# Kernel tuning notes

Measured on AMD Instinct MI355X. Metric: run time of the kernel, lower is better.

Reference implementation:

```python
import jax, jax.numpy as jnp
import numpy as np


@jax.custom_vjp
def sign_ste(x):
    return jnp.sign(x)

def _sign_ste_fwd(x):
    return jnp.sign(x), x

def _sign_ste_bwd(x, g):
    gate = (jnp.abs(x) < 1.0).astype(g.dtype)
    return (g * gate,)

sign_ste.defvjp(_sign_ste_fwd, _sign_ste_bwd)


def setup_inputs() -> dict:
    key = jax.random.key(0)
    ks = jax.random.split(key, 6)
    B, S, D_IN, D_OUT, R = 4, 4096, 4096, 4096, 128
    x = jax.random.normal(ks[0], (B, S, D_IN), dtype=jnp.float32)
    U_latent = jax.random.normal(ks[1], (D_OUT, R), dtype=jnp.float32) * 0.05
    V_latent = jax.random.normal(ks[2], (D_IN, R), dtype=jnp.float32) * 0.05
    s1 = jax.random.uniform(ks[3], (D_OUT,), dtype=jnp.float32, minval=0.01, maxval=0.1)
    s2 = jax.random.uniform(ks[4], (D_IN,), dtype=jnp.float32, minval=0.01, maxval=0.1)
    bias = jax.random.normal(ks[5], (D_OUT,), dtype=jnp.float32) * 0.02
    return {"x": x, "U_latent": U_latent, "V_latent": V_latent, "s1": s1, "s2": s2, "bias": bias}


def reference(x, U_latent, V_latent, s1, s2, bias):
    cdtype = x.dtype
    U_sign = sign_ste(U_latent.astype(cdtype))  # [d_out, r]
    V_sign = sign_ste(V_latent.astype(cdtype))  # [d_in, r]
    z = x * s2.astype(cdtype)                   # [..., d_in]
    z = z @ V_sign                               # [..., r]
    z = z @ U_sign.T                             # [..., d_out]
    z = z * s1.astype(cdtype)
    z = z + bias.astype(cdtype)
    return z
```

## Files before the change

kernel.cpp:

```cpp
#include <hip/hip_runtime.h>

typedef float f32x4 __attribute__((ext_vector_type(4)));
typedef _Float16 f16x8 __attribute__((ext_vector_type(8)));
typedef __fp16 fp16x2 __attribute__((ext_vector_type(2)));

#define M_TOT 16384
#define K_IN  4096
#define R_DIM 128
#define N_OUT 4096

__device__ __forceinline__ _Float16 sign_f16(float v) {
  return v > 0.f ? (_Float16)1.f : (v < 0.f ? (_Float16)-1.f : (_Float16)0.f);
}

__device__ __forceinline__ void cvt8v(f32x4 a, f32x4 b, f16x8& h, f16x8& l) {
#pragma unroll
  for (int j = 0; j < 2; ++j) {
    fp16x2 h0 = __builtin_amdgcn_cvt_pkrtz(a[2 * j], a[2 * j + 1]);
    fp16x2 h1 = __builtin_amdgcn_cvt_pkrtz(b[2 * j], b[2 * j + 1]);
    fp16x2 l0 = __builtin_amdgcn_cvt_pkrtz(a[2 * j] - (float)h0[0], a[2 * j + 1] - (float)h0[1]);
    fp16x2 l1 = __builtin_amdgcn_cvt_pkrtz(b[2 * j] - (float)h1[0], b[2 * j + 1] - (float)h1[1]);
    h[2 * j] = (_Float16)h0[0]; h[2 * j + 1] = (_Float16)h0[1];
    h[4 + 2 * j] = (_Float16)h1[0]; h[5 + 2 * j] = (_Float16)h1[1];
    l[2 * j] = (_Float16)l0[0]; l[2 * j + 1] = (_Float16)l0[1];
    l[4 + 2 * j] = (_Float16)l1[0]; l[5 + 2 * j] = (_Float16)l1[1];
  }
}

__device__ __forceinline__ void gload16(const void* g, void* l) {
  __builtin_amdgcn_global_load_lds((const __attribute__((address_space(1))) unsigned int*)g,
                                   (__attribute__((address_space(3))) unsigned int*)l, 16, 0, 0);
}

__global__ __launch_bounds__(256)
void k_prep(const float* __restrict__ U, const float* __restrict__ V,
            _Float16* __restrict__ VsT_sw, _Float16* __restrict__ Us) {
  __shared__ _Float16 tl[128 * 72];
  const int t = threadIdx.x;
  const int b = blockIdx.x;

  {
    size_t base = (size_t)b * 2048 + (size_t)t * 8;
    f32x4 u0 = *(const f32x4*)(U + base);
    f32x4 u1 = *(const f32x4*)(U + base + 4);
    f16x8 s;
#pragma unroll
    for (int j = 0; j < 4; ++j) { s[j] = sign_f16(u0[j]); s[j + 4] = sign_f16(u1[j]); }
    *(f16x8*)(Us + base) = s;
  }

  if (b < 64) {
#pragma unroll
    for (int it = 0; it < 8; ++it) {
      int idx4 = it * 256 + t;
      int kl = idx4 >> 5;
      int r4 = (idx4 & 31) * 4;
      f32x4 v = *(const f32x4*)(V + (size_t)(b * 64 + kl) * R_DIM + r4);
#pragma unroll
      for (int j = 0; j < 4; ++j) tl[(r4 + j) * 72 + kl] = sign_f16(v[j]);
    }
    __syncthreads();
#pragma unroll
    for (int c = 0; c < 4; ++c) {
      int off = t * 64 + c * 16;
      int r = off >> 7;
      int cB = (off & 127) ^ ((r & 7) << 4);
      f16x8 o = *(const f16x8*)(tl + r * 72 + (cB >> 1));
      *(f16x8*)((char*)VsT_sw + (size_t)b * 16384 + off) = o;
    }
  }
}

#define LOADX(T, X0, X1, X2, X3, S0, S1, S2, S3)            \
  {                                                          \
    X0 = *(const f32x4*)(xp + (T) * 64);                     \
    X1 = *(const f32x4*)(xp + (T) * 64 + 4);                 \
    X2 = *(const f32x4*)(xp + (T) * 64 + 32);                \
    X3 = *(const f32x4*)(xp + (T) * 64 + 36);                \
    S0 = *(const f32x4*)(sp + (T) * 64);                     \
    S1 = *(const f32x4*)(sp + (T) * 64 + 4);                 \
    S2 = *(const f32x4*)(sp + (T) * 64 + 32);                \
    S3 = *(const f32x4*)(sp + (T) * 64 + 36);                \
  }

#define K1BODY(T, X0, X1, X2, X3, S0, S1, S2, S3, Y0, Y1, Y2, Y3, R0, R1, R2, R3) \
  {                                                                                \
    f16x8 ah0, al0, ah1, al1;                                                      \
    cvt8v(X0 * S0, X1 * S1, ah0, al0);                                             \
    cvt8v(X2 * S2, X3 * S3, ah1, al1);                                             \
    if ((T) < 63) {                                                                \
      const char* src = (const char*)VsT_sw + (size_t)((T) + 1) * 16384 +          \
                        wave * 1024 + lane * 16;                                   \
      char* dst = smem + (((T) + 1) & 1) * 16384 + wave * 1024;                    \
      gload16(src, dst);                                                           \
      gload16(src + 8192, dst + 8192);                                             \
      LOADX((T) + 1, Y0, Y1, Y2, Y3, R0, R1, R2, R3);                              \
    }                                                                              \
    const char* bb = smem + ((T) & 1) * 16384;                                     \
    f16x8 b00 = *(const f16x8*)(bb + brow0 * 128 + ((kq16) ^ bsw0));               \
    f16x8 b01 = *(const f16x8*)(bb + brow0 * 128 + ((64 + kq16) ^ bsw0));          \
    f16x8 b10 = *(const f16x8*)(bb + brow1 * 128 + ((kq16) ^ bsw1));               \
    f16x8 b11 = *(const f16x8*)(bb + brow1 * 128 + ((64 + kq16) ^ bsw1));          \
    acc0 = __builtin_amdgcn_mfma_f32_16x16x32_f16(ah0, b00, acc0, 0, 0, 0);        \
    acc0 = __builtin_amdgcn_mfma_f32_16x16x32_f16(al0, b00, acc0, 0, 0, 0);        \
    acc0 = __builtin_amdgcn_mfma_f32_16x16x32_f16(ah1, b01, acc0, 0, 0, 0);        \
    acc0 = __builtin_amdgcn_mfma_f32_16x16x32_f16(al1, b01, acc0, 0, 0, 0);        \
    acc1 = __builtin_amdgcn_mfma_f32_16x16x32_f16(ah0, b10, acc1, 0, 0, 0);        \
    acc1 = __builtin_amdgcn_mfma_f32_16x16x32_f16(al0, b10, acc1, 0, 0, 0);        \
    acc1 = __builtin_amdgcn_mfma_f32_16x16x32_f16(ah1, b11, acc1, 0, 0, 0);        \
    acc1 = __builtin_amdgcn_mfma_f32_16x16x32_f16(al1, b11, acc1, 0, 0, 0);        \
    __syncthreads();                                                               \
  }

__global__ __launch_bounds__(512, 4)
void k1_z(const float* __restrict__ x, const float* __restrict__ s2,
          const _Float16* __restrict__ VsT_sw,
          _Float16* __restrict__ Zswh, _Float16* __restrict__ Zswl) {
  __shared__ char smem[32768];
  const int t = threadIdx.x;
  const int lane = t & 63;
  const int wave = t >> 6;
  const int m0 = blockIdx.x * 32;
  const int wr = wave & 1, wc = wave >> 1;

  const int kq8 = (lane >> 4) * 8;
  const int kq16 = (lane >> 4) * 16;
  const int arow = m0 + wr * 16 + (lane & 15);
  const float* xp = x + (size_t)arow * K_IN + kq8;
  const float* sp = s2 + kq8;

  const int brow0 = wc * 32 + (lane & 15);
  const int brow1 = brow0 + 16;
  const int bsw0 = (brow0 & 7) << 4;
  const int bsw1 = (brow1 & 7) << 4;

  f32x4 acc0 = {0.f, 0.f, 0.f, 0.f};
  f32x4 acc1 = {0.f, 0.f, 0.f, 0.f};

  {
    const char* src = (const char*)VsT_sw + wave * 1024 + lane * 16;
    char* dst = smem + wave * 1024;
    gload16(src, dst);
    gload16(src + 8192, dst + 8192);
  }
  f32x4 xa0, xa1, xa2, xa3, sa0, sa1, sa2, sa3;
  f32x4 xb0, xb1, xb2, xb3, sb0, sb1, sb2, sb3;
  LOADX(0, xa0, xa1, xa2, xa3, sa0, sa1, sa2, sa3);
  __syncthreads();

  for (int tt = 0; tt < 32; ++tt) {
    const int t0 = tt * 2;
    K1BODY(t0,     xa0, xa1, xa2, xa3, sa0, sa1, sa2, sa3,
                   xb0, xb1, xb2, xb3, sb0, sb1, sb2, sb3);
    K1BODY(t0 + 1, xb0, xb1, xb2, xb3, sb0, sb1, sb2, sb3,
                   xa0, xa1, xa2, xa3, sa0, sa1, sa2, sa3);
  }

  float* ZT = (float*)smem;
#pragma unroll
  for (int j = 0; j < 4; ++j) {
    ZT[(wr * 16 + (lane >> 4) * 4 + j) * 132 + wc * 32 + (lane & 15)]      = acc0[j];
    ZT[(wr * 16 + (lane >> 4) * 4 + j) * 132 + wc * 32 + 16 + (lane & 15)] = acc1[j];
  }
  __syncthreads();
  {
    const int lr = t >> 4;
    const int c0 = (t & 15) * 8;
    f32x4 v0 = *(const f32x4*)(ZT + lr * 132 + c0);
    f32x4 v1 = *(const f32x4*)(ZT + lr * 132 + c0 + 4);
    f16x8 h, l;
    cvt8v(v0, v1, h, l);
    const int sw = (lr & 7) << 4;
    const int m = m0 + lr;
    *(f16x8*)((char*)Zswh + (size_t)m * 256 + ((c0 * 2) ^ sw)) = h;
    *(f16x8*)((char*)Zswl + (size_t)m * 256 + ((c0 * 2) ^ sw)) = l;
  }
}

__global__ __launch_bounds__(256, 4)
void k2_out(const _Float16* __restrict__ Zswh, const _Float16* __restrict__ Zswl,
            const _Float16* __restrict__ Us, const float* __restrict__ s1,
            const float* __restrict__ bias, float* __restrict__ out) {
  __shared__ char smem[32768];
  const int t = threadIdx.x;
  const int lane = t & 63;
  const int wave = t >> 6;
  const int bid = blockIdx.x;
  const int nb = bid & 31;
  const int mb = bid >> 5;
  const int m0 = mb * 64, n0 = nb * 128;
  const int wm = wave & 1, wn = wave >> 1;

  f16x8 bf[4][4];
#pragma unroll
  for (int ks = 0; ks < 4; ++ks)
#pragma unroll
    for (int nf = 0; nf < 4; ++nf) {
      const int n = n0 + wn * 64 + nf * 16 + (lane & 15);
      bf[ks][nf] = *(const f16x8*)(Us + (size_t)n * R_DIM + ks * 32 + (lane >> 4) * 8);
    }

  const char* gh = (const char*)Zswh + (size_t)m0 * 256;
  const char* gl = (const char*)Zswl + (size_t)m0 * 256;
#pragma unroll
  for (int q = 0; q < 4; ++q) {
    gload16(gh + wave * 1024 + q * 4096 + lane * 16, smem + wave * 1024 + q * 4096);
    gload16(gl + wave * 1024 + q * 4096 + lane * 16, smem + 16384 + wave * 1024 + q * 4096);
  }
  __syncthreads();

  f32x4 acc[2][4] = {};
  const int kq = (lane >> 4) * 16;
#pragma unroll
  for (int mf = 0; mf < 2; ++mf) {
    const int lr = wm * 32 + mf * 16 + (lane & 15);
    const int sw = (lr & 7) << 4;
#pragma unroll
    for (int ks = 0; ks < 4; ++ks) {
      const int cb = (ks * 64 + kq) ^ sw;
      f16x8 ah = *(const f16x8*)(smem + lr * 256 + cb);
      f16x8 al = *(const f16x8*)(smem + 16384 + lr * 256 + cb);
#pragma unroll
      for (int nf = 0; nf < 4; ++nf) {
        acc[mf][nf] = __builtin_amdgcn_mfma_f32_16x16x32_f16(ah, bf[ks][nf], acc[mf][nf], 0, 0, 0);
        acc[mf][nf] = __builtin_amdgcn_mfma_f32_16x16x32_f16(al, bf[ks][nf], acc[mf][nf], 0, 0, 0);
      }
    }
  }

#pragma unroll
  for (int nf = 0; nf < 4; ++nf) {
    const int col = n0 + wn * 64 + nf * 16 + (lane & 15);
    const float sv = s1[col];
    const float bv = bias[col];
#pragma unroll
    for (int mf = 0; mf < 2; ++mf) {
      const int row = m0 + wm * 32 + mf * 16 + (lane >> 4) * 4;
#pragma unroll
      for (int j = 0; j < 4; ++j)
        out[(size_t)(row + j) * N_OUT + col] = acc[mf][nf][j] * sv + bv;
    }
  }
}

extern "C" void kernel_launch(void* const* d_in, const int* in_sizes, int n_in,
                              void* d_out, int out_size, void* d_ws, size_t ws_size,
                              hipStream_t stream) {
  const float* x    = (const float*)d_in[0];
  const float* U    = (const float*)d_in[1];
  const float* V    = (const float*)d_in[2];
  const float* s1   = (const float*)d_in[3];
  const float* s2   = (const float*)d_in[4];
  const float* bias = (const float*)d_in[5];
  float* out = (float*)d_out;

  char* w = (char*)d_ws;
  _Float16* VsT_sw = (_Float16*)(w);
  _Float16* Us     = (_Float16*)(w + (1 << 20));
  _Float16* Zswh   = (_Float16*)(w + (2 << 20));
  _Float16* Zswl   = (_Float16*)(w + (6 << 20));

  k_prep<<<dim3(256), dim3(256), 0, stream>>>(U, V, VsT_sw, Us);
  k1_z<<<dim3(512), dim3(512), 0, stream>>>(x, s2, VsT_sw, Zswh, Zswl);
  k2_out<<<dim3(8192), dim3(256), 0, stream>>>(Zswh, Zswl, Us, s1, bias, out);
}
```

Baseline: 607.4 us.

## Split k1 reduction over K across waves with register-resident B and partial-sum reduce kernel

The first GEMM (x*s2 @ sign(V)) is restructured so each 256-thread block handles 16 rows, with each wave covering a quarter of K and all 128 output columns. B fragments are loaded directly from a plain row-major transposed VsT in global memory into registers, replacing the LDS double buffering and per-step __syncthreads. Four partial Z results are written in fp32 to a new workspace and summed by a new k1r kernel, which also performs the hi/lo fp16 split and swizzle. This removes block-level synchronisation and doubles the grid, at the cost of extra global traffic for the partials, an extra launch, and redundant B reads from global/L2.

```diff
diff --git a/kernel.cpp b/kernel.cpp
--- a/kernel.cpp
+++ b/kernel.cpp
@@ -34,7 +34,7 @@
 
 __global__ __launch_bounds__(256)
 void k_prep(const float* __restrict__ U, const float* __restrict__ V,
-            _Float16* __restrict__ VsT_sw, _Float16* __restrict__ Us) {
+            _Float16* __restrict__ VsT, _Float16* __restrict__ Us) {
   __shared__ _Float16 tl[128 * 72];
   const int t = threadIdx.x;
   const int b = blockIdx.x;
@@ -60,121 +60,128 @@
       for (int j = 0; j < 4; ++j) tl[(r4 + j) * 72 + kl] = sign_f16(v[j]);
     }
     __syncthreads();
-#pragma unroll
-    for (int c = 0; c < 4; ++c) {
-      int off = t * 64 + c * 16;
-      int r = off >> 7;
-      int cB = (off & 127) ^ ((r & 7) << 4);
-      f16x8 o = *(const f16x8*)(tl + r * 72 + (cB >> 1));
-      *(f16x8*)((char*)VsT_sw + (size_t)b * 16384 + off) = o;
-    }
-  }
-}
-
-#define LOADX(T, X0, X1, X2, X3, S0, S1, S2, S3)            \
-  {                                                          \
-    X0 = *(const f32x4*)(xp + (T) * 64);                     \
-    X1 = *(const f32x4*)(xp + (T) * 64 + 4);                 \
-    X2 = *(const f32x4*)(xp + (T) * 64 + 32);                \
-    X3 = *(const f32x4*)(xp + (T) * 64 + 36);                \
-    S0 = *(const f32x4*)(sp + (T) * 64);                     \
-    S1 = *(const f32x4*)(sp + (T) * 64 + 4);                 \
-    S2 = *(const f32x4*)(sp + (T) * 64 + 32);                \
-    S3 = *(const f32x4*)(sp + (T) * 64 + 36);                \
-  }
-
-#define K1BODY(T, X0, X1, X2, X3, S0, S1, S2, S3, Y0, Y1, Y2, Y3, R0, R1, R2, R3) \
-  {                                                                                \
-    f16x8 ah0, al0, ah1, al1;                                                      \
-    cvt8v(X0 * S0, X1 * S1, ah0, al0);                                             \
-    cvt8v(X2 * S2, X3 * S3, ah1, al1);                                             \
-    if ((T) < 63) {                                                                \
-      const char* src = (const char*)VsT_sw + (size_t)((T) + 1) * 16384 +          \
-                        wave * 1024 + lane * 16;                                   \
-      char* dst = smem + (((T) + 1) & 1) * 16384 + wave * 1024;                    \
-      gload16(src, dst);                                                           \
-      gload16(src + 8192, dst + 8192);                                             \
-      LOADX((T) + 1, Y0, Y1, Y2, Y3, R0, R1, R2, R3);                              \
-    }                                                                              \
-    const char* bb = smem + ((T) & 1) * 16384;                                     \
-    f16x8 b00 = *(const f16x8*)(bb + brow0 * 128 + ((kq16) ^ bsw0));               \
-    f16x8 b01 = *(const f16x8*)(bb + brow0 * 128 + ((64 + kq16) ^ bsw0));          \
-    f16x8 b10 = *(const f16x8*)(bb + brow1 * 128 + ((kq16) ^ bsw1));               \
-    f16x8 b11 = *(const f16x8*)(bb + brow1 * 128 + ((64 + kq16) ^ bsw1));          \
-    acc0 = __builtin_amdgcn_mfma_f32_16x16x32_f16(ah0, b00, acc0, 0, 0, 0);        \
-    acc0 = __builtin_amdgcn_mfma_f32_16x16x32_f16(al0, b00, acc0, 0, 0, 0);        \
-    acc0 = __builtin_amdgcn_mfma_f32_16x16x32_f16(ah1, b01, acc0, 0, 0, 0);        \
-    acc0 = __builtin_amdgcn_mfma_f32_16x16x32_f16(al1, b01, acc0, 0, 0, 0);        \
-    acc1 = __builtin_amdgcn_mfma_f32_16x16x32_f16(ah0, b10, acc1, 0, 0, 0);        \
-    acc1 = __builtin_amdgcn_mfma_f32_16x16x32_f16(al0, b10, acc1, 0, 0, 0);        \
-    acc1 = __builtin_amdgcn_mfma_f32_16x16x32_f16(ah1, b11, acc1, 0, 0, 0);        \
-    acc1 = __builtin_amdgcn_mfma_f32_16x16x32_f16(al1, b11, acc1, 0, 0, 0);        \
-    __syncthreads();                                                               \
-  }
-
-__global__ __launch_bounds__(512, 4)
+    {
+      const int r = t >> 1;
+      const int kh = (t & 1) * 32;
+#pragma unroll
+      for (int j = 0; j < 4; ++j) {
+        f16x8 o = *(const f16x8*)(tl + r * 72 + kh + j * 8);
+        *(f16x8*)(VsT + (size_t)r * K_IN + b * 64 + kh + j * 8) = o;
+      }
+    }
+  }
+}
+
+#define K1LOAD(T, X0, X1, S0, S1, B0, B1, B2, B3, B4, B5, B6, B7) \
+  {                                                               \
+    const int koff = (T) * 32;                                    \
+    X0 = *(const f32x4*)(xp + koff);                              \
+    X1 = *(const f32x4*)(xp + koff + 4);                          \
+    S0 = *(const f32x4*)(sp + koff);                              \
+    S1 = *(const f32x4*)(sp + koff + 4);                          \
+    B0 = *(const f16x8*)(bp0 + koff);                             \
+    B1 = *(const f16x8*)(bp1 + koff);                             \
+    B2 = *(const f16x8*)(bp2 + koff);                             \
+    B3 = *(const f16x8*)(bp3 + koff);                             \
+    B4 = *(const f16x8*)(bp4 + koff);                             \
+    B5 = *(const f16x8*)(bp5 + koff);                             \
+    B6 = *(const f16x8*)(bp6 + koff);                             \
+    B7 = *(const f16x8*)(bp7 + koff);                             \
+  }
+
+#define K1COMP(X0, X1, S0, S1, B0, B1, B2, B3, B4, B5, B6, B7)          \
+  {                                                                     \
+    f16x8 ah, al;                                                       \
+    cvt8v(X0 * S0, X1 * S1, ah, al);                                    \
+    acc0 = __builtin_amdgcn_mfma_f32_16x16x32_f16(ah, B0, acc0, 0, 0, 0); \
+    acc0 = __builtin_amdgcn_mfma_f32_16x16x32_f16(al, B0, acc0, 0, 0, 0); \
+    acc1 = __builtin_amdgcn_mfma_f32_16x16x32_f16(ah, B1, acc1, 0, 0, 0); \
+    acc1 = __builtin_amdgcn_mfma_f32_16x16x32_f16(al, B1, acc1, 0, 0, 0); \
+    acc2 = __builtin_amdgcn_mfma_f32_16x16x32_f16(ah, B2, acc2, 0, 0, 0); \
+    acc2 = __builtin_amdgcn_mfma_f32_16x16x32_f16(al, B2, acc2, 0, 0, 0); \
+    acc3 = __builtin_amdgcn_mfma_f32_16x16x32_f16(ah, B3, acc3, 0, 0, 0); \
+    acc3 = __builtin_amdgcn_mfma_f32_16x16x32_f16(al, B3, acc3, 0, 0, 0); \
+    acc4 = __builtin_amdgcn_mfma_f32_16x16x32_f16(ah, B4, acc4, 0, 0, 0); \
+    acc4 = __builtin_amdgcn_mfma_f32_16x16x32_f16(al, B4, acc4, 0, 0, 0); \
+    acc5 = __builtin_amdgcn_mfma_f32_16x16x32_f16(ah, B5, acc5, 0, 0, 0); \
+    acc5 = __builtin_amdgcn_mfma_f32_16x16x32_f16(al, B5, acc5, 0, 0, 0); \
+    acc6 = __builtin_amdgcn_mfma_f32_16x16x32_f16(ah, B6, acc6, 0, 0, 0); \
+    acc6 = __builtin_amdgcn_mfma_f32_16x16x32_f16(al, B6, acc6, 0, 0, 0); \
+    acc7 = __builtin_amdgcn_mfma_f32_16x16x32_f16(ah, B7, acc7, 0, 0, 0); \
+    acc7 = __builtin_amdgcn_mfma_f32_16x16x32_f16(al, B7, acc7, 0, 0, 0); \
+  }
+
+__global__ __launch_bounds__(256, 2)
 void k1_z(const float* __restrict__ x, const float* __restrict__ s2,
-          const _Float16* __restrict__ VsT_sw,
-          _Float16* __restrict__ Zswh, _Float16* __restrict__ Zswl) {
-  __shared__ char smem[32768];
+          const _Float16* __restrict__ VsT, float* __restrict__ Z4) {
   const int t = threadIdx.x;
   const int lane = t & 63;
-  const int wave = t >> 6;
-  const int m0 = blockIdx.x * 32;
-  const int wr = wave & 1, wc = wave >> 1;
-
+  const int q = t >> 6;
+  const int m0 = blockIdx.x * 16;
+  const int k0 = q * 1024;
   const int kq8 = (lane >> 4) * 8;
-  const int kq16 = (lane >> 4) * 16;
-  const int arow = m0 + wr * 16 + (lane & 15);
-  const float* xp = x + (size_t)arow * K_IN + kq8;
-  const float* sp = s2 + kq8;
-
-  const int brow0 = wc * 32 + (lane & 15);
-  const int brow1 = brow0 + 16;
-  const int bsw0 = (brow0 & 7) << 4;
-  const int bsw1 = (brow1 & 7) << 4;
-
-  f32x4 acc0 = {0.f, 0.f, 0.f, 0.f};
-  f32x4 acc1 = {0.f, 0.f, 0.f, 0.f};
-
-  {
-    const char* src = (const char*)VsT_sw + wave * 1024 + lane * 16;
-    char* dst = smem + wave * 1024;
-    gload16(src, dst);
-    gload16(src + 8192, dst + 8192);
-  }
-  f32x4 xa0, xa1, xa2, xa3, sa0, sa1, sa2, sa3;
-  f32x4 xb0, xb1, xb2, xb3, sb0, sb1, sb2, sb3;
-  LOADX(0, xa0, xa1, xa2, xa3, sa0, sa1, sa2, sa3);
-  __syncthreads();
-
-  for (int tt = 0; tt < 32; ++tt) {
-    const int t0 = tt * 2;
-    K1BODY(t0,     xa0, xa1, xa2, xa3, sa0, sa1, sa2, sa3,
-                   xb0, xb1, xb2, xb3, sb0, sb1, sb2, sb3);
-    K1BODY(t0 + 1, xb0, xb1, xb2, xb3, sb0, sb1, sb2, sb3,
-                   xa0, xa1, xa2, xa3, sa0, sa1, sa2, sa3);
-  }
-
-  float* ZT = (float*)smem;
-#pragma unroll
-  for (int j = 0; j < 4; ++j) {
-    ZT[(wr * 16 + (lane >> 4) * 4 + j) * 132 + wc * 32 + (lane & 15)]      = acc0[j];
-    ZT[(wr * 16 + (lane >> 4) * 4 + j) * 132 + wc * 32 + 16 + (lane & 15)] = acc1[j];
-  }
-  __syncthreads();
-  {
-    const int lr = t >> 4;
-    const int c0 = (t & 15) * 8;
-    f32x4 v0 = *(const f32x4*)(ZT + lr * 132 + c0);
-    f32x4 v1 = *(const f32x4*)(ZT + lr * 132 + c0 + 4);
-    f16x8 h, l;
-    cvt8v(v0, v1, h, l);
-    const int sw = (lr & 7) << 4;
-    const int m = m0 + lr;
-    *(f16x8*)((char*)Zswh + (size_t)m * 256 + ((c0 * 2) ^ sw)) = h;
-    *(f16x8*)((char*)Zswl + (size_t)m * 256 + ((c0 * 2) ^ sw)) = l;
-  }
+  const int lcol = lane & 15;
+
+  const float* xp = x + (size_t)(m0 + lcol) * K_IN + k0 + kq8;
+  const float* sp = s2 + k0 + kq8;
+  const _Float16* bb = VsT + (size_t)lcol * K_IN + k0 + kq8;
+  const _Float16* bp0 = bb;
+  const _Float16* bp1 = bb + (size_t)16 * K_IN;
+  const _Float16* bp2 = bb + (size_t)32 * K_IN;
+  const _Float16* bp3 = bb + (size_t)48 * K_IN;
+  const _Float16* bp4 = bb + (size_t)64 * K_IN;
+  const _Float16* bp5 = bb + (size_t)80 * K_IN;
+  const _Float16* bp6 = bb + (size_t)96 * K_IN;
+  const _Float16* bp7 = bb + (size_t)112 * K_IN;
+
+  f32x4 acc0 = {0.f,0.f,0.f,0.f}, acc1 = acc0, acc2 = acc0, acc3 = acc0;
+  f32x4 acc4 = acc0, acc5 = acc0, acc6 = acc0, acc7 = acc0;
+
+  f32x4 xA0, xA1, sA0, sA1, xB0, xB1, sB0, sB1;
+  f16x8 bA0, bA1, bA2, bA3, bA4, bA5, bA6, bA7;
+  f16x8 bB0, bB1, bB2, bB3, bB4, bB5, bB6, bB7;
+
+  K1LOAD(0, xA0, xA1, sA0, sA1, bA0, bA1, bA2, bA3, bA4, bA5, bA6, bA7);
+  for (int tt = 0; tt < 16; ++tt) {
+    K1LOAD((tt * 2 + 1) & 31, xB0, xB1, sB0, sB1, bB0, bB1, bB2, bB3, bB4, bB5, bB6, bB7);
+    __builtin_amdgcn_sched_barrier(0);
+    K1COMP(xA0, xA1, sA0, sA1, bA0, bA1, bA2, bA3, bA4, bA5, bA6, bA7);
+    K1LOAD((tt * 2 + 2) & 31, xA0, xA1, sA0, sA1, bA0, bA1, bA2, bA3, bA4, bA5, bA6, bA7);
+    __builtin_amdgcn_sched_barrier(0);
+    K1COMP(xB0, xB1, sB0, sB1, bB0, bB1, bB2, bB3, bB4, bB5, bB6, bB7);
+  }
+
+  float* Zq = Z4 + (size_t)q * M_TOT * R_DIM;
+  const int mrow = m0 + (lane >> 4) * 4;
+#define ZST(FR, ACC)                                                   \
+  _Pragma("unroll")                                                    \
+  for (int j = 0; j < 4; ++j)                                          \
+    Zq[(size_t)(mrow + j) * R_DIM + (FR) * 16 + lcol] = ACC[j];
+  ZST(0, acc0) ZST(1, acc1) ZST(2, acc2) ZST(3, acc3)
+  ZST(4, acc4) ZST(5, acc5) ZST(6, acc6) ZST(7, acc7)
+#undef ZST
+}
+
+__global__ __launch_bounds__(256)
+void k1r(const float* __restrict__ Z4,
+         _Float16* __restrict__ Zswh, _Float16* __restrict__ Zswl) {
+  const int idx = blockIdx.x * 256 + threadIdx.x;
+  const int m = idx >> 4;
+  const int c = (idx & 15) * 8;
+  const float* p = Z4 + (size_t)m * R_DIM + c;
+  const size_t QS = (size_t)M_TOT * R_DIM;
+  f32x4 a0 = *(const f32x4*)(p);
+  f32x4 a1 = *(const f32x4*)(p + 4);
+#pragma unroll
+  for (int qq = 1; qq < 4; ++qq) {
+    a0 += *(const f32x4*)(p + qq * QS);
+    a1 += *(const f32x4*)(p + qq * QS + 4);
+  }
+  f16x8 h, l;
+  cvt8v(a0, a1, h, l);
+  const int sw = (m & 7) << 4;
+  *(f16x8*)((char*)Zswh + (size_t)m * 256 + ((c * 2) ^ sw)) = h;
+  *(f16x8*)((char*)Zswl + (size_t)m * 256 + ((c * 2) ^ sw)) = l;
 }
 
 __global__ __launch_bounds__(256, 4)
@@ -203,9 +210,9 @@
   const char* gh = (const char*)Zswh + (size_t)m0 * 256;
   const char* gl = (const char*)Zswl + (size_t)m0 * 256;
 #pragma unroll
-  for (int q = 0; q < 4; ++q) {
-    gload16(gh + wave * 1024 + q * 4096 + lane * 16, smem + wave * 1024 + q * 4096);
-    gload16(gl + wave * 1024 + q * 4096 + lane * 16, smem + 16384 + wave * 1024 + q * 4096);
+  for (int qq = 0; qq < 4; ++qq) {
+    gload16(gh + wave * 1024 + qq * 4096 + lane * 16, smem + wave * 1024 + qq * 4096);
+    gload16(gl + wave * 1024 + qq * 4096 + lane * 16, smem + 16384 + wave * 1024 + qq * 4096);
   }
   __syncthreads();
 
@@ -255,12 +262,14 @@
   float* out = (float*)d_out;
 
   char* w = (char*)d_ws;
-  _Float16* VsT_sw = (_Float16*)(w);
-  _Float16* Us     = (_Float16*)(w + (1 << 20));
-  _Float16* Zswh   = (_Float16*)(w + (2 << 20));
-  _Float16* Zswl   = (_Float16*)(w + (6 << 20));
-
-  k_prep<<<dim3(256), dim3(256), 0, stream>>>(U, V, VsT_sw, Us);
-  k1_z<<<dim3(512), dim3(512), 0, stream>>>(x, s2, VsT_sw, Zswh, Zswl);
+  _Float16* VsT  = (_Float16*)(w);
+  _Float16* Us   = (_Float16*)(w + (1 << 20));
+  _Float16* Zswh = (_Float16*)(w + (2 << 20));
+  _Float16* Zswl = (_Float16*)(w + (6 << 20));
+  float*    Z4   = (float*)(w + (10 << 20));
+
+  k_prep<<<dim3(256), dim3(256), 0, stream>>>(U, V, VsT, Us);
+  k1_z<<<dim3(1024), dim3(256), 0, stream>>>(x, s2, VsT, Z4);
+  k1r<<<dim3(1024), dim3(256), 0, stream>>>(Z4, Zswh, Zswl);
   k2_out<<<dim3(8192), dim3(256), 0, stream>>>(Zswh, Zswl, Us, s1, bias, out);
 }
```

After: 615.3 us. No clear change (+1.3%).
